# Kernel tuning notes

Hardware: AMD Instinct MI355X
Metric: run time of the kernel (lower is better)

## Reference

```python
import math
import jax, jax.numpy as jnp
import numpy as np

GRID_SIZE = 17
GRID_RANGE = 2.5
WIDTHS = [128, 256, 128]
LN_EPS = 1e-5

GRID = jnp.linspace(-GRID_RANGE, GRID_RANGE, GRID_SIZE, dtype=jnp.float32)
SPACING = jnp.float32(2.0 * GRID_RANGE / (GRID_SIZE - 1))


def _kan_layer(x, base_scale, spline_w, bias):
    # x: (B, I); base_scale: (I, O); spline_w: (I, O, G); bias: (O,)
    I = x.shape[-1]
    # degree-1 (hat) spline basis: (B, I, G)
    basis = jnp.clip(1.0 - jnp.abs(x[..., None] - GRID) / SPACING, 0.0, None)
    spline = jnp.einsum('big,iog->bio', basis, spline_w)          # (B, I, O)
    base = jax.nn.silu(x)[..., None] * base_scale[None]            # (B, I, O)
    edge = base + spline                                           # (B, I, O)
    out = edge.sum(axis=1) / math.sqrt(float(I)) + bias            # (B, O)
    return out, edge, basis


def _layer_norm(x, gamma, beta):
    mu = x.mean(axis=-1, keepdims=True)
    var = ((x - mu) ** 2).mean(axis=-1, keepdims=True)
    return (x - mu) * jax.lax.rsqrt(var + LN_EPS) * gamma + beta


def setup_inputs() -> dict:
    key = jax.random.key(0)
    ks = jax.random.split(key, 8)
    B = 4096
    I0, H, O = WIDTHS
    fan0 = 1.0 / math.sqrt(float(I0))
    fan1 = 1.0 / math.sqrt(float(H))
    return {
        'x': jax.random.normal(ks[0], (B, I0), dtype=jnp.float32),
        'base_scale0': fan0 * jax.random.normal(ks[1], (I0, H), dtype=jnp.float32),
        'spline_w0': 0.1 * fan0 * jax.random.normal(ks[2], (I0, H, GRID_SIZE), dtype=jnp.float32),
        'bias0': jnp.zeros((H,), dtype=jnp.float32),
        'base_scale1': fan1 * jax.random.normal(ks[3], (H, O), dtype=jnp.float32),
        'spline_w1': 0.1 * fan1 * jax.random.normal(ks[4], (H, O, GRID_SIZE), dtype=jnp.float32),
        'bias1': jnp.zeros((O,), dtype=jnp.float32),
        'ln_gamma': jnp.ones((H,), dtype=jnp.float32),
        'ln_beta': jnp.zeros((H,), dtype=jnp.float32),
    }


def reference(x, base_scale0, spline_w0, bias0, base_scale1, spline_w1, bias1, ln_gamma, ln_beta):
    h, _, _ = _kan_layer(x, base_scale0, spline_w0, bias0)
    h = _layer_norm(h, ln_gamma, ln_beta)
    out, edge1, basis1 = _kan_layer(h, base_scale1, spline_w1, bias1)
    # diagnostics on the last layer (mean/std, std unbiased=False)
    se_mean = edge1.mean()
    se_std = edge1.std()
    sb_mean = basis1.mean()
    sb_std = basis1.std()
    return out, edge1, basis1, se_mean, se_std, sb_mean, sb_std
```

## Files before the change

kernel.cpp:

```cpp
#include <hip/hip_runtime.h>

#define BATCH 4096
#define NI 128
#define NH 256
#define NO 128
#define NG 17
#define GM_ROWS 8

static constexpr size_t EDGE_OFF  = (size_t)BATCH * NO;
static constexpr size_t BASIS_OFF = EDGE_OFF + (size_t)BATCH * NH * NO;
static constexpr size_t SCAL_OFF  = BASIS_OFF + (size_t)BATCH * NH * NG;

typedef float  vf2 __attribute__((ext_vector_type(2)));
typedef float  vf4 __attribute__((ext_vector_type(4)));

__device__ __forceinline__ unsigned short f2bf(float v) {
    unsigned int b = __float_as_uint(v);
    b += 0x7FFFu + ((b >> 16) & 1u);
    return (unsigned short)(b >> 16);
}
__device__ __forceinline__ float2 bf2_to_f2(unsigned int v) {
    float2 r;
    r.x = __uint_as_float(v << 16);
    r.y = __uint_as_float(v & 0xFFFF0000u);
    return r;
}
__device__ __forceinline__ float4 bf4_to_f4(uint2 v) {
    float4 r;
    r.x = __uint_as_float(v.x << 16);
    r.y = __uint_as_float(v.x & 0xFFFF0000u);
    r.z = __uint_as_float(v.y << 16);
    r.w = __uint_as_float(v.y & 0xFFFF0000u);
    return r;
}

__device__ __forceinline__ void taps(float v, float& sil, float& wlo, float& whi,
                                     int& glo, int& ghi, float& u) {
    sil = v / (1.0f + __expf(-v));
    u   = (v + 2.5f) * 3.2f;
    float kf = floorf(u);
    int   k  = (int)kf;
    float f  = u - kf;
    wlo = 1.0f - f;  whi = f;
    glo = k;         ghi = k + 1;
    if (glo < 0 || glo > 16) { glo = 0; wlo = 0.0f; }
    if (ghi < 0 || ghi > 16) { ghi = 0; whi = 0.0f; }
}

__global__ __launch_bounds__(256) void transpose_convert(
    const float* __restrict__ w0, const float* __restrict__ w1,
    const float* __restrict__ bs1,
    unsigned short* __restrict__ w0t, unsigned short* __restrict__ w1t,
    unsigned short* __restrict__ bs1b) {
    int j = blockIdx.x * 256 + threadIdx.x;
    const int total0 = NI * NG * NH;
    const int total1 = NH * NG * NO;
    if (j < total0) {
        int i = j / (NG * NH);
        int r = j - i * (NG * NH);
        int g = r / NH;
        int o = r - g * NH;
        w0t[j] = f2bf(w0[((size_t)i * NH + o) * NG + g]);
    } else if (j < total0 + total1) {
        int jj = j - total0;
        int i = jj / (NG * NO);
        int r = jj - i * (NG * NO);
        int g = r / NO;
        int o = r - g * NO;
        w1t[jj] = f2bf(w1[((size_t)i * NO + o) * NG + g]);
    } else {
        int jj = j - total0 - total1;
        bs1b[jj] = f2bf(bs1[jj]);
    }
}

__global__ __launch_bounds__(256) void base_gemm(
    const float* __restrict__ x,
    const float* __restrict__ bs0,
    float* __restrict__ hbase)
{
    __shared__ float s_sil[GM_ROWS * NI];
    const int tid = threadIdx.x;
    const int rb  = blockIdx.x * GM_ROWS;

    #pragma unroll
    for (int j = tid; j < GM_ROWS * NI; j += 256) {
        float xv = x[(size_t)rb * NI + j];
        s_sil[j] = xv / (1.0f + __expf(-xv));
    }
    __syncthreads();

    float acc[GM_ROWS] = {};
    const int o = tid;
    #pragma unroll 4
    for (int k = 0; k < NI; ++k) {
        float bv = bs0[(size_t)k * NH + o];
        #pragma unroll
        for (int r = 0; r < GM_ROWS; ++r)
            acc[r] += s_sil[r * NI + k] * bv;
    }
    #pragma unroll
    for (int r = 0; r < GM_ROWS; ++r)
        hbase[(size_t)(rb + r) * NH + o] = acc[r];
}

__global__ __launch_bounds__(128) void kan_fused(
    const float* __restrict__ x,
    const float* __restrict__ hbase,
    const float* __restrict__ bias0,
    const unsigned short* __restrict__ bs1,
    const float* __restrict__ bias1,
    const float* __restrict__ gamma,
    const float* __restrict__ beta,
    const unsigned short* __restrict__ w0t,
    const unsigned short* __restrict__ w1t,
    float* __restrict__ out,
    float4* __restrict__ partials)
{
    __shared__ float s_wlo0[NI], s_whi0[NI];
    __shared__ int   s_gp0[NI];
    __shared__ float s_sil1[NH], s_wlo1[NH], s_whi1[NH], s_u1[NH];
    __shared__ int   s_glo1[NH], s_ghi1[NH];
    __shared__ float2 s_ln[2];
    __shared__ float4 s_out4[128];
    __shared__ float4 s_red4[128];

    const int tid = threadIdx.x;
    const int b   = blockIdx.x;

    {
        float xv = x[(size_t)b * NI + tid];
        float sil, wlo, whi, u; int glo, ghi;
        taps(xv, sil, wlo, whi, glo, ghi, u);
        s_wlo0[tid] = wlo; s_whi0[tid] = whi;
        s_gp0[tid] = glo | (ghi << 8);
    }
    __syncthreads();

    const int op = tid * 2;
    float h0 = 0.0f, h1 = 0.0f;
    #pragma unroll 8
    for (int i = 0; i < NI; ++i) {
        const float wlo = s_wlo0[i], whi = s_whi0[i];
        const unsigned int gp = (unsigned int)s_gp0[i];
        const float2 wl = bf2_to_f2(*reinterpret_cast<const unsigned int*>(w0t + ((size_t)i * NG + (gp & 0xffu)) * NH + op));
        const float2 wh = bf2_to_f2(*reinterpret_cast<const unsigned int*>(w0t + ((size_t)i * NG + (gp >> 8)) * NH + op));
        h0 += wlo * wl.x + whi * wh.x;
        h1 += wlo * wl.y + whi * wh.y;
    }
    {
        const float2 hb = *reinterpret_cast<const float2*>(hbase + (size_t)b * NH + op);
        const float2 b0 = *reinterpret_cast<const float2*>(bias0 + op);
        h0 = (h0 + hb.x) * 0.08838834764831844f + b0.x;
        h1 = (h1 + hb.y) * 0.08838834764831844f + b0.y;
    }

    {
        float s = h0 + h1, q = h0 * h0 + h1 * h1;
        #pragma unroll
        for (int d = 1; d < 64; d <<= 1) {
            s += __shfl_xor(s, d, 64);
            q += __shfl_xor(q, d, 64);
        }
        if ((tid & 63) == 0) s_ln[tid >> 6] = make_float2(s, q);
    }
    __syncthreads();
    float hn0, hn1;
    {
        const float2 a = s_ln[0], c = s_ln[1];
        const float mu = (a.x + c.x) * (1.0f / NH);
        const float ms = (a.y + c.y) * (1.0f / NH);
        const float rs = rsqrtf(ms - mu * mu + 1e-5f);
        const float2 gm = *reinterpret_cast<const float2*>(gamma + op);
        const float2 bt = *reinterpret_cast<const float2*>(beta + op);
        hn0 = (h0 - mu) * rs * gm.x + bt.x;
        hn1 = (h1 - mu) * rs * gm.y + bt.y;
    }

    float bsum, bsq;
    {
        float sil, wlo, whi, u; int glo, ghi;
        taps(hn0, sil, wlo, whi, glo, ghi, u);
        s_sil1[op] = sil; s_wlo1[op] = wlo; s_whi1[op] = whi;
        s_glo1[op] = glo; s_ghi1[op] = ghi; s_u1[op] = u;
        bsum = wlo + whi;  bsq = wlo * wlo + whi * whi;
        taps(hn1, sil, wlo, whi, glo, ghi, u);
        s_sil1[op + 1] = sil; s_wlo1[op + 1] = wlo; s_whi1[op + 1] = whi;
        s_glo1[op + 1] = glo; s_ghi1[op + 1] = ghi; s_u1[op + 1] = u;
        bsum += wlo + whi; bsq += wlo * wlo + whi * whi;
    }
    __syncthreads();

    {
        float* bo = out + BASIS_OFF + (size_t)b * (NH * NG);
        #pragma unroll
        for (int it = 0; it < 17; ++it) {
            int f0 = (it * 128 + tid) * 2;
            int i0 = f0 / NG,       g0 = f0 - i0 * NG;
            int i1 = (f0 + 1) / NG, g1 = (f0 + 1) - i1 * NG;
            vf2 v;
            v.x = fmaxf(0.0f, 1.0f - fabsf(s_u1[i0] - (float)g0));
            v.y = fmaxf(0.0f, 1.0f - fabsf(s_u1[i1] - (float)g1));
            __builtin_nontemporal_store(v, reinterpret_cast<vf2*>(bo + f0));
        }
    }

    const int po = (tid & 31) * 4;
    const int q  = tid >> 5;
    float4 osum = make_float4(0.f, 0.f, 0.f, 0.f);
    float esq = 0.0f;
    float* eo = out + EDGE_OFF + (size_t)b * (NH * NO);
    #pragma unroll 4
    for (int it = 0; it < 64; ++it) {
        const int i = q * 64 + it;
        const float sil = s_sil1[i], wlo = s_wlo1[i], whi = s_whi1[i];
        const float4 bsv = bf4_to_f4(*reinterpret_cast<const uint2*>(bs1 + (size_t)i * NO + po));
        const float4 wl  = bf4_to_f4(*reinterpret_cast<const uint2*>(w1t + (size_t)(i * NG + s_glo1[i]) * NO + po));
        const float4 wh  = bf4_to_f4(*reinterpret_cast<const uint2*>(w1t + (size_t)(i * NG + s_ghi1[i]) * NO + po));
        vf4 e;
        e.x = sil * bsv.x + wlo * wl.x + whi * wh.x;
        e.y = sil * bsv.y + wlo * wl.y + whi * wh.y;
        e.z = sil * bsv.z + wlo * wl.z + whi * wh.z;
        e.w = sil * bsv.w + wlo * wl.w + whi * wh.w;
        __builtin_nontemporal_store(e, reinterpret_cast<vf4*>(eo + (size_t)i * NO + po));
        osum.x += e.x; osum.y += e.y; osum.z += e.z; osum.w += e.w;
        esq += e.x * e.x + e.y * e.y + e.z * e.z + e.w * e.w;
    }

    s_out4[tid] = osum;
    __syncthreads();
    if (tid < 32) {
        float4 a = s_out4[tid], b2 = s_out4[tid + 32], c = s_out4[tid + 64], d2 = s_out4[tid + 96];
        const float4 bi = *reinterpret_cast<const float4*>(bias1 + tid * 4);
        float4 o4;
        o4.x = (a.x + b2.x + c.x + d2.x) * 0.0625f + bi.x;
        o4.y = (a.y + b2.y + c.y + d2.y) * 0.0625f + bi.y;
        o4.z = (a.z + b2.z + c.z + d2.z) * 0.0625f + bi.z;
        o4.w = (a.w + b2.w + c.w + d2.w) * 0.0625f + bi.w;
        *reinterpret_cast<float4*>(out + (size_t)b * NO + tid * 4) = o4;
    }

    s_red4[tid] = make_float4(osum.x + osum.y + osum.z + osum.w, esq, bsum, bsq);
    __syncthreads();
    for (int s = 64; s > 0; s >>= 1) {
        if (tid < s) {
            float4 a = s_red4[tid], c = s_red4[tid + s];
            s_red4[tid] = make_float4(a.x + c.x, a.y + c.y, a.z + c.z, a.w + c.w);
        }
        __syncthreads();
    }
    if (tid == 0) partials[b] = s_red4[0];
}

__global__ __launch_bounds__(256) void finalize(const float4* __restrict__ partials,
                                                float* __restrict__ out) {
    __shared__ double red[256];
    const int tid = threadIdx.x;
    double a0 = 0, a1 = 0, a2 = 0, a3 = 0;
    for (int j = tid; j < BATCH; j += 256) {
        float4 p = partials[j];
        a0 += (double)p.x; a1 += (double)p.y; a2 += (double)p.z; a3 += (double)p.w;
    }
    double tot[4];
    double v[4] = {a0, a1, a2, a3};
    for (int c = 0; c < 4; ++c) {
        red[tid] = v[c];
        __syncthreads();
        for (int s = 128; s > 0; s >>= 1) {
            if (tid < s) red[tid] += red[tid + s];
            __syncthreads();
        }
        tot[c] = red[0];
        __syncthreads();
    }
    if (tid == 0) {
        const double Ne = (double)BATCH * NH * NO;
        const double Nb = (double)BATCH * NH * NG;
        double me = tot[0] / Ne;
        double ve = tot[1] / Ne - me * me;
        double mb = tot[2] / Nb;
        double vb = tot[3] / Nb - mb * mb;
        out[SCAL_OFF + 0] = (float)me;
        out[SCAL_OFF + 1] = (float)sqrt(ve > 0.0 ? ve : 0.0);
        out[SCAL_OFF + 2] = (float)mb;
        out[SCAL_OFF + 3] = (float)sqrt(vb > 0.0 ? vb : 0.0);
    }
}

extern "C" void kernel_launch(void* const* d_in, const int* in_sizes, int n_in,
                              void* d_out, int out_size, void* d_ws, size_t ws_size,
                              hipStream_t stream) {
    const float* x     = (const float*)d_in[0];
    const float* bs0   = (const float*)d_in[1];
    const float* w0    = (const float*)d_in[2];
    const float* bias0 = (const float*)d_in[3];
    const float* bs1   = (const float*)d_in[4];
    const float* w1    = (const float*)d_in[5];
    const float* bias1 = (const float*)d_in[6];
    const float* gamma = (const float*)d_in[7];
    const float* beta  = (const float*)d_in[8];
    float* out = (float*)d_out;

    unsigned short* w0t  = (unsigned short*)d_ws;
    unsigned short* w1t  = w0t + (size_t)NI * NG * NH;
    unsigned short* bs1b = w1t + (size_t)NH * NG * NO;
    size_t ofs = ((size_t)(NI * NG * NH) + (size_t)(NH * NG * NO) + NH * NO) * sizeof(unsigned short);
    ofs = (ofs + 15) & ~(size_t)15;
    float4* partials = (float4*)((char*)d_ws + ofs);
    float*  hbase    = (float*)((char*)d_ws + ofs + BATCH * sizeof(float4));

    hipLaunchKernelGGL(transpose_convert, dim3(4480), dim3(256), 0, stream,
                       w0, w1, bs1, w0t, w1t, bs1b);
    hipLaunchKernelGGL(base_gemm, dim3(BATCH / GM_ROWS), dim3(256), 0, stream,
                       x, bs0, hbase);
    hipLaunchKernelGGL(kan_fused, dim3(BATCH), dim3(128), 0, stream,
                       x, hbase, bias0, bs1b, bias1, gamma, beta, w0t, w1t, out, partials);
    hipLaunchKernelGGL(finalize, dim3(1), dim3(256), 0, stream, partials, out);
}
```

Baseline: 148.2 us.

## Compute layer-0 spline as dense bf16 MFMA GEMM over materialized basis

Layer 0's sparse two-tap gather loop is replaced by a dense GEMM. A per-row bf16 hat-basis matrix (K=128*17) is materialized, and the spline weights are repacked into an MFMA-friendly tiled layout. A new spline_gemm kernel uses 16x16x32 bf16 MFMA and adds its result into the base-term buffer, and the prep kernels are merged into one launch. This trades the scattered weight gathers in kan_fused for about 8x more (dense) flops and an extra round-trip of the basis matrix through memory.

```diff
diff --git a/kernel.cpp b/kernel.cpp
--- a/kernel.cpp
+++ b/kernel.cpp
@@ -6,6 +6,8 @@
 #define NO 128
 #define NG 17
 #define GM_ROWS 8
+#define K0 2176
+#define KU 1088
 
 static constexpr size_t EDGE_OFF  = (size_t)BATCH * NO;
 static constexpr size_t BASIS_OFF = EDGE_OFF + (size_t)BATCH * NH * NO;
@@ -13,17 +15,13 @@
 
 typedef float  vf2 __attribute__((ext_vector_type(2)));
 typedef float  vf4 __attribute__((ext_vector_type(4)));
+typedef short  bf16x8 __attribute__((ext_vector_type(8)));
+typedef float  f32x4 __attribute__((ext_vector_type(4)));
 
 __device__ __forceinline__ unsigned short f2bf(float v) {
     unsigned int b = __float_as_uint(v);
     b += 0x7FFFu + ((b >> 16) & 1u);
     return (unsigned short)(b >> 16);
-}
-__device__ __forceinline__ float2 bf2_to_f2(unsigned int v) {
-    float2 r;
-    r.x = __uint_as_float(v << 16);
-    r.y = __uint_as_float(v & 0xFFFF0000u);
-    return r;
 }
 __device__ __forceinline__ float4 bf4_to_f4(uint2 v) {
     float4 r;
@@ -47,78 +45,129 @@
     if (ghi < 0 || ghi > 16) { ghi = 0; whi = 0.0f; }
 }
 
-__global__ __launch_bounds__(256) void transpose_convert(
+__global__ __launch_bounds__(256) void prep_all(
+    const float* __restrict__ x,
     const float* __restrict__ w0, const float* __restrict__ w1,
-    const float* __restrict__ bs1,
-    unsigned short* __restrict__ w0t, unsigned short* __restrict__ w1t,
-    unsigned short* __restrict__ bs1b) {
-    int j = blockIdx.x * 256 + threadIdx.x;
-    const int total0 = NI * NG * NH;
-    const int total1 = NH * NG * NO;
-    if (j < total0) {
-        int i = j / (NG * NH);
-        int r = j - i * (NG * NH);
-        int g = r / NH;
-        int o = r - g * NH;
-        w0t[j] = f2bf(w0[((size_t)i * NH + o) * NG + g]);
-    } else if (j < total0 + total1) {
-        int jj = j - total0;
-        int i = jj / (NG * NO);
-        int r = jj - i * (NG * NO);
-        int g = r / NO;
-        int o = r - g * NO;
-        w1t[jj] = f2bf(w1[((size_t)i * NO + o) * NG + g]);
+    const float* __restrict__ bs1, const float* __restrict__ bs0,
+    unsigned short* __restrict__ w0B, unsigned short* __restrict__ w1t,
+    unsigned short* __restrict__ bs1b,
+    unsigned int* __restrict__ basisA, float* __restrict__ hbase)
+{
+    __shared__ float s_u[NI];
+    __shared__ float s_sil[GM_ROWS * NI];
+    const int blk = blockIdx.x;
+    const int tid = threadIdx.x;
+
+    if (blk < 2372) {
+        int j = blk * 256 + tid;
+        const int n0 = 68 * NH;
+        const int total1 = NH * NG * NO;
+        if (j < n0) {
+            const int kt = j >> 8;
+            const int o  = j & 255;
+            unsigned short* dst = w0B + (size_t)kt * 8192 + o * 32;
+            #pragma unroll
+            for (int kl = 0; kl < 32; ++kl) {
+                unsigned int k = kt * 32 + kl;
+                unsigned int i = (k * 3856u) >> 16;
+                unsigned int g = k - 17u * i;
+                dst[kl] = f2bf(w0[((size_t)i * NH + o) * NG + g]);
+            }
+        } else if (j < n0 + total1) {
+            int jj = j - n0;
+            int i = jj / (NG * NO);
+            int r = jj - i * (NG * NO);
+            int g = r / NO;
+            int o = r - g * NO;
+            w1t[jj] = f2bf(w1[((size_t)i * NO + o) * NG + g]);
+        } else if (j < n0 + total1 + NH * NO) {
+            int jj = j - n0 - total1;
+            bs1b[jj] = f2bf(bs1[jj]);
+        }
+    } else if (blk < 2372 + BATCH) {
+        const int b = blk - 2372;
+        if (tid < NI) {
+            float xv = x[(size_t)b * NI + tid];
+            s_u[tid] = (xv + 2.5f) * 3.2f;
+        }
+        __syncthreads();
+        unsigned int* dst = basisA + (size_t)b * KU;
+        #pragma unroll
+        for (int c = 0; c < 5; ++c) {
+            int idx = c * 256 + tid;
+            if (idx < KU) {
+                unsigned int k0 = idx * 2u, k1 = idx * 2u + 1u;
+                unsigned int i0 = (k0 * 3856u) >> 16, g0 = k0 - 17u * i0;
+                unsigned int i1 = (k1 * 3856u) >> 16, g1 = k1 - 17u * i1;
+                float v0 = fmaxf(0.0f, 1.0f - fabsf(s_u[i0] - (float)g0));
+                float v1 = fmaxf(0.0f, 1.0f - fabsf(s_u[i1] - (float)g1));
+                dst[idx] = (unsigned int)f2bf(v0) | ((unsigned int)f2bf(v1) << 16);
+            }
+        }
     } else {
-        int jj = j - total0 - total1;
-        bs1b[jj] = f2bf(bs1[jj]);
-    }
-}
-
-__global__ __launch_bounds__(256) void base_gemm(
-    const float* __restrict__ x,
-    const float* __restrict__ bs0,
-    float* __restrict__ hbase)
+        const int rb = (blk - 2372 - BATCH) * GM_ROWS;
+        #pragma unroll
+        for (int j = tid; j < GM_ROWS * NI; j += 256) {
+            float xv = x[(size_t)rb * NI + j];
+            s_sil[j] = xv / (1.0f + __expf(-xv));
+        }
+        __syncthreads();
+        float acc[GM_ROWS] = {};
+        const int o = tid;
+        #pragma unroll 4
+        for (int k = 0; k < NI; ++k) {
+            float bv = bs0[(size_t)k * NH + o];
+            #pragma unroll
+            for (int r = 0; r < GM_ROWS; ++r)
+                acc[r] += s_sil[r * NI + k] * bv;
+        }
+        #pragma unroll
+        for (int r = 0; r < GM_ROWS; ++r)
+            hbase[(size_t)(rb + r) * NH + o] = acc[r];
+    }
+}
+
+__global__ __launch_bounds__(256) void spline_gemm(
+    const unsigned short* __restrict__ basisA,
+    const unsigned short* __restrict__ w0B,
+    float* __restrict__ hsum)
 {
-    __shared__ float s_sil[GM_ROWS * NI];
-    const int tid = threadIdx.x;
-    const int rb  = blockIdx.x * GM_ROWS;
-
+    const int bm   = blockIdx.x & 255;
+    const int bn   = blockIdx.x >> 8;
+    const int tid  = threadIdx.x;
+    const int lane = tid & 63;
+    const int wave = tid >> 6;
+    const int r    = lane & 15;
+    const int kg   = lane >> 4;
+    const int o    = bn * 64 + wave * 16 + r;
+
+    const unsigned short* arow  = basisA + (size_t)(bm * 16 + r) * K0 + kg * 8;
+    const unsigned short* bbase = w0B + (size_t)o * 32 + kg * 8;
+    f32x4 acc = {0.f, 0.f, 0.f, 0.f};
+    #pragma unroll 4
+    for (int kt = 0; kt < 68; ++kt) {
+        const bf16x8 av = *reinterpret_cast<const bf16x8*>(arow + kt * 32);
+        const bf16x8 bv = *reinterpret_cast<const bf16x8*>(bbase + (size_t)kt * 8192);
+        acc = __builtin_amdgcn_mfma_f32_16x16x32_bf16(av, bv, acc, 0, 0, 0);
+    }
     #pragma unroll
-    for (int j = tid; j < GM_ROWS * NI; j += 256) {
-        float xv = x[(size_t)rb * NI + j];
-        s_sil[j] = xv / (1.0f + __expf(-xv));
-    }
-    __syncthreads();
-
-    float acc[GM_ROWS] = {};
-    const int o = tid;
-    #pragma unroll 4
-    for (int k = 0; k < NI; ++k) {
-        float bv = bs0[(size_t)k * NH + o];
-        #pragma unroll
-        for (int r = 0; r < GM_ROWS; ++r)
-            acc[r] += s_sil[r * NI + k] * bv;
-    }
-    #pragma unroll
-    for (int r = 0; r < GM_ROWS; ++r)
-        hbase[(size_t)(rb + r) * NH + o] = acc[r];
+    for (int reg = 0; reg < 4; ++reg) {
+        const size_t idx = (size_t)(bm * 16 + kg * 4 + reg) * NH + o;
+        hsum[idx] += acc[reg];
+    }
 }
 
 __global__ __launch_bounds__(128) void kan_fused(
-    const float* __restrict__ x,
-    const float* __restrict__ hbase,
+    const float* __restrict__ hsum,
     const float* __restrict__ bias0,
     const unsigned short* __restrict__ bs1,
     const float* __restrict__ bias1,
     const float* __restrict__ gamma,
     const float* __restrict__ beta,
-    const unsigned short* __restrict__ w0t,
     const unsigned short* __restrict__ w1t,
     float* __restrict__ out,
     float4* __restrict__ partials)
 {
-    __shared__ float s_wlo0[NI], s_whi0[NI];
-    __shared__ int   s_gp0[NI];
     __shared__ float s_sil1[NH], s_wlo1[NH], s_whi1[NH], s_u1[NH];
     __shared__ int   s_glo1[NH], s_ghi1[NH];
     __shared__ float2 s_ln[2];
@@ -128,31 +177,13 @@
     const int tid = threadIdx.x;
     const int b   = blockIdx.x;
 
-    {
-        float xv = x[(size_t)b * NI + tid];
-        float sil, wlo, whi, u; int glo, ghi;
-        taps(xv, sil, wlo, whi, glo, ghi, u);
-        s_wlo0[tid] = wlo; s_whi0[tid] = whi;
-        s_gp0[tid] = glo | (ghi << 8);
-    }
-    __syncthreads();
-
     const int op = tid * 2;
-    float h0 = 0.0f, h1 = 0.0f;
-    #pragma unroll 8
-    for (int i = 0; i < NI; ++i) {
-        const float wlo = s_wlo0[i], whi = s_whi0[i];
-        const unsigned int gp = (unsigned int)s_gp0[i];
-        const float2 wl = bf2_to_f2(*reinterpret_cast<const unsigned int*>(w0t + ((size_t)i * NG + (gp & 0xffu)) * NH + op));
-        const float2 wh = bf2_to_f2(*reinterpret_cast<const unsigned int*>(w0t + ((size_t)i * NG + (gp >> 8)) * NH + op));
-        h0 += wlo * wl.x + whi * wh.x;
-        h1 += wlo * wl.y + whi * wh.y;
-    }
-    {
-        const float2 hb = *reinterpret_cast<const float2*>(hbase + (size_t)b * NH + op);
+    float h0, h1;
+    {
+        const float2 hs = *reinterpret_cast<const float2*>(hsum + (size_t)b * NH + op);
         const float2 b0 = *reinterpret_cast<const float2*>(bias0 + op);
-        h0 = (h0 + hb.x) * 0.08838834764831844f + b0.x;
-        h1 = (h1 + hb.y) * 0.08838834764831844f + b0.y;
+        h0 = hs.x * 0.08838834764831844f + b0.x;
+        h1 = hs.y * 0.08838834764831844f + b0.y;
     }
 
     {
@@ -301,19 +332,20 @@
     const float* beta  = (const float*)d_in[8];
     float* out = (float*)d_out;
 
-    unsigned short* w0t  = (unsigned short*)d_ws;
-    unsigned short* w1t  = w0t + (size_t)NI * NG * NH;
+    unsigned short* w0B  = (unsigned short*)d_ws;
+    unsigned short* w1t  = w0B + (size_t)68 * 8192;
     unsigned short* bs1b = w1t + (size_t)NH * NG * NO;
-    size_t ofs = ((size_t)(NI * NG * NH) + (size_t)(NH * NG * NO) + NH * NO) * sizeof(unsigned short);
+    size_t ofs = ((size_t)(68 * 8192) + (size_t)(NH * NG * NO) + NH * NO) * sizeof(unsigned short);
     ofs = (ofs + 15) & ~(size_t)15;
-    float4* partials = (float4*)((char*)d_ws + ofs);
-    float*  hbase    = (float*)((char*)d_ws + ofs + BATCH * sizeof(float4));
-
-    hipLaunchKernelGGL(transpose_convert, dim3(4480), dim3(256), 0, stream,
-                       w0, w1, bs1, w0t, w1t, bs1b);
-    hipLaunchKernelGGL(base_gemm, dim3(BATCH / GM_ROWS), dim3(256), 0, stream,
-                       x, bs0, hbase);
+    float4*       partials = (float4*)((char*)d_ws + ofs);
+    float*        hsum     = (float*)((char*)d_ws + ofs + BATCH * sizeof(float4));
+    unsigned int* basisA   = (unsigned int*)(hsum + (size_t)BATCH * NH);
+
+    hipLaunchKernelGGL(prep_all, dim3(2372 + BATCH + BATCH / GM_ROWS), dim3(256), 0, stream,
+                       x, w0, w1, bs1, bs0, w0B, w1t, bs1b, basisA, hsum);
+    hipLaunchKernelGGL(spline_gemm, dim3(1024), dim3(256), 0, stream,
+                       (const unsigned short*)basisA, w0B, hsum);
     hipLaunchKernelGGL(kan_fused, dim3(BATCH), dim3(128), 0, stream,
-                       x, hbase, bias0, bs1b, bias1, gamma, beta, w0t, w1t, out, partials);
+                       hsum, bias0, bs1b, bias1, gamma, beta, w1t, out, partials);
     hipLaunchKernelGGL(finalize, dim3(1), dim3(256), 0, stream, partials, out);
 }
```

Measured after the change: 180.7 us. 1.22x slower.
